# Performance work log

Measured on AMD Instinct MI355X. Metric: run time of the kernel, lower is better.

Reference implementation:

```python
import jax, jax.numpy as jnp
import numpy as np

D = 65
CHUNK = 64
K = 64
SCALE = D ** (-0.5)

def gelu(x):
    return jax.nn.gelu(x, approximate=False)  # torch nn.GELU default is exact erf

def setup_inputs() -> dict:
    key = jax.random.key(0)
    ks = jax.random.split(key, 16)
    B, N = 32, 16384
    s = SCALE
    return {
        "x": jax.random.normal(ks[0], (B, N, D), jnp.float32),
        # query_gen: Linear(D,D) -> GELU -> Linear(D, K*D)
        "Wq1": jax.random.normal(ks[1], (D, D), jnp.float32) * s,
        "bq1": jnp.zeros((D,), jnp.float32),
        "Wq2": jax.random.normal(ks[2], (D, K * D), jnp.float32) * s,
        "bq2": jnp.zeros((K * D,), jnp.float32),
        "Wk": jax.random.normal(ks[3], (D, D), jnp.float32) * s,
        "bk": jnp.zeros((D,), jnp.float32),
        "Wv": jax.random.normal(ks[4], (D, D), jnp.float32) * s,
        "bv": jnp.zeros((D,), jnp.float32),
        "cross_q": jax.random.normal(ks[5], (1, D), jnp.float32) * s,
        "pos_enc": jax.random.normal(ks[6], (1, CHUNK, D), jnp.float32) * s,
        "Wr": jax.random.normal(ks[7], (D, D), jnp.float32) * (1.0 / np.sqrt(D)),
        "br": jnp.zeros((D,), jnp.float32),
        "gamma": jnp.ones((D,), jnp.float32),
        "beta": jnp.zeros((D,), jnp.float32),
    }

def reference(x, Wq1, bq1, Wq2, bq2, Wk, bk, Wv, bv, cross_q, pos_enc, Wr, br, gamma, beta):
    B, N, d = x.shape
    nb = N // CHUNK  # N chosen divisible by CHUNK -> mask is all True, pad branch skipped

    # global average (mask all-ones => plain mean over N)
    gavg = jnp.mean(x, axis=1)  # [B, D]

    # queries: MLP on global average, reshape to [B, K, D], scaled
    q = (gelu(gavg @ Wq1 + bq1) @ Wq2 + bq2).reshape(B, K, d) * SCALE

    # keys / values: Linear + GELU, chunked, + positional encoding per chunk
    keys = gelu(x @ Wk + bk).reshape(B, nb, CHUNK, d) + pos_enc[None]      # [B,nb,C,D]
    values = gelu(x @ Wv + bv).reshape(B, nb, CHUNK, d) + pos_enc[None]    # [B,nb,C,D]

    # block-local attention (mask is all-True, masked_fill is a no-op)
    scores = jnp.einsum('bkd,bncd->bnkc', q, keys) * SCALE                 # [B,nb,K,C]
    w = jax.nn.softmax(scores, axis=-1)                                    # dropout = eval-mode identity
    blk = jnp.einsum('bnkc,bncd->bnkd', w, values)                         # [B,nb,K,D]
    blk = jnp.transpose(blk, (0, 2, 1, 3))                                 # [B,K,nb,D]

    # cross-block attention with a single learned query
    cs = jnp.einsum('d,bknd->bkn', cross_q[0], blk) * SCALE                # [B,K,nb]
    cw = jax.nn.softmax(cs, axis=-1)
    compressed = jnp.einsum('bkn,bknd->bkd', cw, blk)                      # [B,K,D]

    # residual + LayerNorm
    compressed = compressed + (gavg @ Wr + br)[:, None, :]
    mu = jnp.mean(compressed, axis=-1, keepdims=True)
    var = jnp.var(compressed, axis=-1, keepdims=True)
    return (compressed - mu) * jax.lax.rsqrt(var + 1e-5) * gamma + beta
```

## Files before the change

kernel.cpp:

```cpp
#include <hip/hip_runtime.h>
#include <hip/hip_bf16.h>

#define BATCH 32
#define NSEQ  16384
#define DDIM  65
#define CHUNK 64
#define KQ    64
#define NBLK  256
#define SCALE 0.12403473458920847f

typedef __bf16 bf16x8 __attribute__((ext_vector_type(8)));
typedef float  f32x4  __attribute__((ext_vector_type(4)));
#define MFMA16(a, b, c) __builtin_amdgcn_mfma_f32_16x16x32_bf16(a, b, c, 0, 0, 0)

__device__ __forceinline__ float gelu_exact(float v) {
    return 0.5f * v * (1.0f + erff(v * 0.7071067811865476f));
}

__device__ __forceinline__ float gelu_tanh(float x) {
    float x2 = x * x;
    float t  = 0.7978845608028654f * x * fmaf(0.044715f, x2, 1.0f);
    float e  = __expf(2.0f * t);
    float th = 1.0f - 2.0f * __builtin_amdgcn_rcpf(e + 1.0f);
    return 0.5f * x * (1.0f + th);
}

__global__ __launch_bounds__(256) void k_prep(const float* __restrict__ Wk,
                                              const float* __restrict__ Wv,
                                              __bf16* __restrict__ WkT,
                                              __bf16* __restrict__ WvT) {
    int i = blockIdx.x * 256 + threadIdx.x;
    if (i >= 2 * 80 * 64) return;
    int m = i / 5120;
    int j = i - m * 5120;
    int d = j >> 6, e = j & 63;
    const float* W = m ? Wv : Wk;
    __bf16* T = m ? WvT : WkT;
    T[(size_t)d * 64 + e] = (d < DDIM) ? (__bf16)W[e * DDIM + d] : (__bf16)0.0f;
}

__global__ __launch_bounds__(256) void k_gavg(const float* __restrict__ x,
                                              float* __restrict__ partial) {
    const int s = blockIdx.x;
    const int b = blockIdx.y;
    const int tid = threadIdx.x;
    const int w = tid >> 6, lane = tid & 63;
    const float* xb = x + (size_t)b * NSEQ * DDIM;
    const int n0 = s * 256;
    float acc = 0.f, acce = 0.f;
    #pragma unroll 4
    for (int i = 0; i < 64; ++i) {
        const float* row = xb + (size_t)(n0 + w + i * 4) * DDIM;
        acc  += row[lane];
        acce += row[64];
    }
    __shared__ float part[4][DDIM];
    part[w][lane] = acc;
    if (lane == 0) part[w][64] = acce;
    __syncthreads();
    if (tid < DDIM) {
        partial[((size_t)b * 64 + s) * DDIM + tid] =
            part[0][tid] + part[1][tid] + part[2][tid] + part[3][tid];
    }
}

__global__ __launch_bounds__(256) void k_qgen1(const float* __restrict__ partial,
    const float* __restrict__ Wq1, const float* __restrict__ bq1,
    const float* __restrict__ Wr,  const float* __restrict__ br,
    float* __restrict__ h_out, float* __restrict__ r_out) {
    const int b = blockIdx.x, tid = threadIdx.x;
    __shared__ float g[DDIM];
    if (tid < DDIM) {
        float a = 0.f;
        const float* p = partial + (size_t)b * 64 * DDIM + tid;
        #pragma unroll 8
        for (int s = 0; s < 64; ++s) a += p[s * DDIM];
        g[tid] = a * (1.0f / 16384.0f);
    }
    __syncthreads();
    if (tid < DDIM) {
        float a = bq1[tid];
        for (int e = 0; e < DDIM; ++e) a += g[e] * Wq1[e * DDIM + tid];
        h_out[b * DDIM + tid] = gelu_exact(a);
    } else if (tid >= 128 && tid < 128 + DDIM) {
        const int d = tid - 128;
        float a = br[d];
        for (int e = 0; e < DDIM; ++e) a += g[e] * Wr[e * DDIM + d];
        r_out[b * DDIM + d] = a;
    }
}

__global__ __launch_bounds__(256) void k_qgen2(const float* __restrict__ h_in,
    const float* __restrict__ Wq2, const float* __restrict__ bq2,
    __bf16* __restrict__ qbf, float* __restrict__ q64) {
    const int b = blockIdx.y, tid = threadIdx.x;
    const int o = blockIdx.x * 256 + tid;
    __shared__ float h[DDIM];
    if (tid < DDIM) h[tid] = h_in[b * DDIM + tid];
    __syncthreads();
    if (o >= KQ * DDIM) return;
    float a = bq2[o];
    #pragma unroll 13
    for (int e = 0; e < DDIM; ++e) a += h[e] * Wq2[e * (KQ * DDIM) + o];
    a *= SCALE;
    const int k = o / DDIM, d = o - k * DDIM;
    if (d < 64) qbf[(size_t)b * 4096 + k * 64 + d] = (__bf16)a;
    else        q64[b * 64 + k] = a;
}

__global__ __launch_bounds__(256, 5) void k_attn(const float* __restrict__ x,
    const __bf16* __restrict__ qbf, const float* __restrict__ q64,
    const __bf16* __restrict__ WkT, const __bf16* __restrict__ WvT,
    const float* __restrict__ Wk, const float* __restrict__ bkb,
    const float* __restrict__ Wv, const float* __restrict__ bvb,
    const float* __restrict__ pos, const float* __restrict__ cq,
    __bf16* __restrict__ blk_out, float* __restrict__ cs_out) {
    const int nb = blockIdx.x;
    const int b  = blockIdx.y;
    const int tid = threadIdx.x;
    const int lane = tid & 63, w = tid >> 6;
    const int l16 = lane & 15, quad = lane >> 4;

    __shared__ __align__(16) __bf16 xsP[64 * 72];
    __shared__ __align__(16) __bf16 keys[64 * 72];
    __shared__ __align__(16) __bf16 valsT[64 * 72];
    __shared__ float vals64[64];
    __shared__ float xs64[64];

    {
        const int c = tid >> 2, g = tid & 3;
        const float* xrow = x + ((size_t)b * NSEQ + (size_t)nb * CHUNK + c) * DDIM;
        __bf16* dst = xsP + c * 72;
        #pragma unroll
        for (int j = 0; j < 16; ++j)
            dst[g + 4 * j] = (__bf16)xrow[g + 4 * j];
        if (g == 0) xs64[c] = xrow[64];
    }
    __syncthreads();

    {
        const __bf16* arow = xsP + (w * 16 + l16) * 72 + quad * 8;
        bf16x8 a0 = *(const bf16x8*)arow;
        bf16x8 a1 = *(const bf16x8*)(arow + 32);
        f32x4 ak[5], av[5];
        const f32x4 z = {0.f, 0.f, 0.f, 0.f};
        #pragma unroll
        for (int nt = 0; nt < 5; ++nt) {
            const __bf16* bkr = WkT + (nt * 16 + l16) * 64 + quad * 8;
            const __bf16* bvr = WvT + (nt * 16 + l16) * 64 + quad * 8;
            ak[nt] = MFMA16(a0, *(const bf16x8*)bkr, z);
            ak[nt] = MFMA16(a1, *(const bf16x8*)(bkr + 32), ak[nt]);
            av[nt] = MFMA16(a0, *(const bf16x8*)bvr, z);
            av[nt] = MFMA16(a1, *(const bf16x8*)(bvr + 32), av[nt]);
        }
        float xe[4];
        #pragma unroll
        for (int r = 0; r < 4; ++r) xe[r] = xs64[w * 16 + quad * 4 + r];
        #pragma unroll
        for (int nt = 0; nt < 5; ++nt) {
            const int d = nt * 16 + l16;
            if (d <= 64) {
                const float wk64d = Wk[64 * DDIM + d];
                const float wv64d = Wv[64 * DDIM + d];
                const float bkd = bkb[d], bvd = bvb[d];
                #pragma unroll
                for (int r = 0; r < 4; ++r) {
                    const int c = w * 16 + quad * 4 + r;
                    const float pv = pos[c * DDIM + d];
                    const float kvv = gelu_tanh(ak[nt][r] + xe[r] * wk64d + bkd) + pv;
                    const float vvv = gelu_tanh(av[nt][r] + xe[r] * wv64d + bvd) + pv;
                    keys[c * 72 + d] = (__bf16)kvv;
                    if (d < 64) valsT[d * 72 + c] = (__bf16)vvv;
                    else        vals64[c] = vvv;
                }
            }
        }
    }
    __syncthreads();

    float csr[4];
    {
        const __bf16* aq = qbf + (size_t)b * 4096 + (w * 16 + l16) * 64 + quad * 8;
        bf16x8 qa0 = *(const bf16x8*)aq;
        bf16x8 qa1 = *(const bf16x8*)(aq + 32);
        const f32x4 z = {0.f, 0.f, 0.f, 0.f};
        float st[4][4];
        #pragma unroll
        for (int nt = 0; nt < 4; ++nt) {
            const __bf16* kb = keys + (nt * 16 + l16) * 72 + quad * 8;
            f32x4 sacc = MFMA16(qa0, *(const bf16x8*)kb, z);
            sacc = MFMA16(qa1, *(const bf16x8*)(kb + 32), sacc);
            const float k64c = (float)keys[(nt * 16 + l16) * 72 + 64];
            #pragma unroll
            for (int r = 0; r < 4; ++r) st[nt][r] = sacc[r] * SCALE + 0.f * k64c;
            #pragma unroll
            for (int r = 0; r < 4; ++r)
                st[nt][r] = sacc[r];
            #pragma unroll
            for (int r = 0; r < 4; ++r)
                st[nt][r] = fmaf(q64[b * 64 + w * 16 + quad * 4 + r], k64c,
                                 st[nt][r]) * SCALE;
        }
        float mr[4], sum[4], inv[4];
        #pragma unroll
        for (int r = 0; r < 4; ++r) {
            float m = fmaxf(fmaxf(st[0][r], st[1][r]), fmaxf(st[2][r], st[3][r]));
            m = fmaxf(m, __shfl_xor(m, 1));
            m = fmaxf(m, __shfl_xor(m, 2));
            m = fmaxf(m, __shfl_xor(m, 4));
            m = fmaxf(m, __shfl_xor(m, 8));
            mr[r] = m;
            sum[r] = 0.f;
        }
        #pragma unroll
        for (int nt = 0; nt < 4; ++nt)
            #pragma unroll
            for (int r = 0; r < 4; ++r) {
                st[nt][r] = __expf(st[nt][r] - mr[r]);
                sum[r] += st[nt][r];
            }
        #pragma unroll
        for (int r = 0; r < 4; ++r) {
            float s = sum[r];
            s += __shfl_xor(s, 1);
            s += __shfl_xor(s, 2);
            s += __shfl_xor(s, 4);
            s += __shfl_xor(s, 8);
            inv[r] = __builtin_amdgcn_rcpf(s);
        }
        #pragma unroll
        for (int nt = 0; nt < 4; ++nt)
            #pragma unroll
            for (int r = 0; r < 4; ++r)
                xsP[(w * 16 + quad * 4 + r) * 72 + nt * 16 + l16] =
                    (__bf16)(st[nt][r] * inv[r]);
        float v64l[4];
        #pragma unroll
        for (int nt = 0; nt < 4; ++nt) v64l[nt] = vals64[nt * 16 + l16];
        const float cq64 = cq[64];
        #pragma unroll
        for (int r = 0; r < 4; ++r) {
            float o = st[0][r] * v64l[0];
            o = fmaf(st[1][r], v64l[1], o);
            o = fmaf(st[2][r], v64l[2], o);
            o = fmaf(st[3][r], v64l[3], o);
            o += __shfl_xor(o, 1);
            o += __shfl_xor(o, 2);
            o += __shfl_xor(o, 4);
            o += __shfl_xor(o, 8);
            csr[r] = 0.f;
            if (l16 == 0) {
                const float o64 = o * inv[r];
                const int k = w * 16 + quad * 4 + r;
                blk_out[(((size_t)b * KQ + k) * NBLK + nb) * DDIM + 64] =
                    (__bf16)o64;
                csr[r] = o64 * cq64;
            }
        }
    }
    __syncthreads();

    {
        const __bf16* pr = xsP + (w * 16 + l16) * 72 + quad * 8;
        bf16x8 pa0 = *(const bf16x8*)pr;
        bf16x8 pa1 = *(const bf16x8*)(pr + 32);
        const f32x4 z = {0.f, 0.f, 0.f, 0.f};
        #pragma unroll
        for (int nt = 0; nt < 4; ++nt) {
            const __bf16* vb = valsT + (nt * 16 + l16) * 72 + quad * 8;
            f32x4 o = MFMA16(pa0, *(const bf16x8*)vb, z);
            o = MFMA16(pa1, *(const bf16x8*)(vb + 32), o);
            const int d = nt * 16 + l16;
            const float cqd = cq[d];
            #pragma unroll
            for (int r = 0; r < 4; ++r) {
                const int k = w * 16 + quad * 4 + r;
                blk_out[(((size_t)b * KQ + k) * NBLK + nb) * DDIM + d] =
                    (__bf16)o[r];
                csr[r] = fmaf(o[r], cqd, csr[r]);
            }
        }
        #pragma unroll
        for (int r = 0; r < 4; ++r) {
            float v = csr[r];
            v += __shfl_xor(v, 1);
            v += __shfl_xor(v, 2);
            v += __shfl_xor(v, 4);
            v += __shfl_xor(v, 8);
            if (l16 == 0) {
                const int k = w * 16 + quad * 4 + r;
                cs_out[((size_t)b * KQ + k) * NBLK + nb] = v * SCALE;
            }
        }
    }
}

__global__ __launch_bounds__(256) void k_cross(
    const __bf16* __restrict__ blk, const float* __restrict__ cs,
    const float* __restrict__ r, const float* __restrict__ gamma,
    const float* __restrict__ beta, float* __restrict__ out) {
    const int bk_ = blockIdx.x;
    const int b = bk_ >> 6;
    const int tid = threadIdx.x;
    const int w = tid >> 6, lane = tid & 63;

    __shared__ float ew[NBLK];
    __shared__ float red[4][DDIM];
    __shared__ float vv[DDIM];
    __shared__ float wredA[4];
    __shared__ float stats[2];

    const float v = cs[(size_t)bk_ * NBLK + tid];
    float m = v;
    for (int off = 32; off; off >>= 1) m = fmaxf(m, __shfl_down(m, off));
    if (lane == 0) wredA[w] = m;
    __syncthreads();
    m = fmaxf(fmaxf(wredA[0], wredA[1]), fmaxf(wredA[2], wredA[3]));
    const float e = __expf(v - m);
    ew[tid] = e;
    float s = e;
    for (int off = 32; off; off >>= 1) s += __shfl_down(s, off);
    __syncthreads();
    if (lane == 0) wredA[w] = s;
    __syncthreads();
    const float inv = 1.0f / (wredA[0] + wredA[1] + wredA[2] + wredA[3]);

    const __bf16* base = blk + (size_t)bk_ * NBLK * DDIM;
    float acc = 0.f, acce = 0.f;
    #pragma unroll 4
    for (int i = 0; i < 64; ++i) {
        const int n = w + i * 4;
        const __bf16* row = base + n * DDIM;
        const float wgt = ew[n];
        acc  += wgt * (float)row[lane];
        acce += wgt * (float)row[64];
    }
    red[w][lane] = acc;
    if (lane == 0) red[w][64] = acce;
    __syncthreads();
    if (tid < DDIM) {
        vv[tid] = (red[0][tid] + red[1][tid] + red[2][tid] + red[3][tid]) * inv
                  + r[b * DDIM + tid];
    }
    __syncthreads();
    if (tid < 64) {
        float a  = vv[tid] + (tid == 0 ? vv[64] : 0.f);
        float sq = vv[tid] * vv[tid] + (tid == 0 ? vv[64] * vv[64] : 0.f);
        for (int off = 32; off; off >>= 1) {
            a  += __shfl_down(a, off);
            sq += __shfl_down(sq, off);
        }
        if (tid == 0) {
            const float mu  = a * (1.0f / DDIM);
            const float var = sq * (1.0f / DDIM) - mu * mu;
            stats[0] = mu;
            stats[1] = rsqrtf(var + 1e-5f);
        }
    }
    __syncthreads();
    if (tid < DDIM) {
        out[(size_t)bk_ * DDIM + tid] =
            (vv[tid] - stats[0]) * stats[1] * gamma[tid] + beta[tid];
    }
}

extern "C" void kernel_launch(void* const* d_in, const int* in_sizes, int n_in,
                              void* d_out, int out_size, void* d_ws, size_t ws_size,
                              hipStream_t stream) {
    const float* x    = (const float*)d_in[0];
    const float* Wq1  = (const float*)d_in[1];
    const float* bq1  = (const float*)d_in[2];
    const float* Wq2  = (const float*)d_in[3];
    const float* bq2  = (const float*)d_in[4];
    const float* Wk   = (const float*)d_in[5];
    const float* bk   = (const float*)d_in[6];
    const float* Wv   = (const float*)d_in[7];
    const float* bv   = (const float*)d_in[8];
    const float* cq   = (const float*)d_in[9];
    const float* pos  = (const float*)d_in[10];
    const float* Wr   = (const float*)d_in[11];
    const float* br   = (const float*)d_in[12];
    const float* gamma= (const float*)d_in[13];
    const float* beta = (const float*)d_in[14];
    float* out = (float*)d_out;

    char* w8 = (char*)d_ws;
    float*  partial = (float*)w8;
    float*  rres    = (float*)(w8 + 532480);
    float*  q64     = (float*)(w8 + 540800);
    float*  hbuf    = (float*)(w8 + 548992);
    float*  cs      = (float*)(w8 + 557312);
    __bf16* qbf     = (__bf16*)(w8 + 2654464);
    __bf16* WkT     = (__bf16*)(w8 + 2916608);
    __bf16* WvT     = (__bf16*)(w8 + 2926848);
    __bf16* blk     = (__bf16*)(w8 + 2937088);

    k_prep<<<40, 256, 0, stream>>>(Wk, Wv, WkT, WvT);
    k_gavg<<<dim3(64, BATCH), 256, 0, stream>>>(x, partial);
    k_qgen1<<<BATCH, 256, 0, stream>>>(partial, Wq1, bq1, Wr, br, hbuf, rres);
    k_qgen2<<<dim3(17, BATCH), 256, 0, stream>>>(hbuf, Wq2, bq2, qbf, q64);
    k_attn<<<dim3(NBLK, BATCH), 256, 0, stream>>>(x, qbf, q64, WkT, WvT,
                                                  Wk, bk, Wv, bv, pos, cq,
                                                  blk, cs);
    k_cross<<<BATCH * KQ, 256, 0, stream>>>(blk, cs, rres, gamma, beta, out);
}
```

Measured before the change: 378.3 us.

## Pre-convert x to swizzled bf16 and restructure attention kernel with async LDS loads

The global-average kernel now also writes x as a bf16, XOR-swizzled 64-column copy plus a separate fp32 column 64. The attention kernel pulls this with global_load_lds straight into LDS and uses swizzled unpadded LDS tiles with transposed MFMA operand order so each lane owns one query row, which removes cross-lane softmax reductions and one barrier. The block output layout becomes [b][nb][k] with stride 68 so stores are vectorized, and occupancy is raised to 6. In exchange there is an extra bf16 write and read of x through global memory, and k_cross now reads strided rows.

```diff
diff --git a/kernel.cpp b/kernel.cpp
--- a/kernel.cpp
+++ b/kernel.cpp
@@ -8,8 +8,10 @@
 #define KQ    64
 #define NBLK  256
 #define SCALE 0.12403473458920847f
+#define BSTRIDE 68
 
 typedef __bf16 bf16x8 __attribute__((ext_vector_type(8)));
+typedef __bf16 bf16x4 __attribute__((ext_vector_type(4)));
 typedef float  f32x4  __attribute__((ext_vector_type(4)));
 #define MFMA16(a, b, c) __builtin_amdgcn_mfma_f32_16x16x32_bf16(a, b, c, 0, 0, 0)
 
@@ -23,6 +25,12 @@
     float e  = __expf(2.0f * t);
     float th = 1.0f - 2.0f * __builtin_amdgcn_rcpf(e + 1.0f);
     return 0.5f * x * (1.0f + th);
+}
+
+__device__ __forceinline__ void load_lds16(const void* g, void* l) {
+    __builtin_amdgcn_global_load_lds(
+        (const __attribute__((address_space(1))) unsigned int*)g,
+        (__attribute__((address_space(3))) unsigned int*)l, 16, 0, 0);
 }
 
 __global__ __launch_bounds__(256) void k_prep(const float* __restrict__ Wk,
@@ -40,7 +48,9 @@
 }
 
 __global__ __launch_bounds__(256) void k_gavg(const float* __restrict__ x,
-                                              float* __restrict__ partial) {
+                                              float* __restrict__ partial,
+                                              __bf16* __restrict__ xbf,
+                                              float* __restrict__ x64g) {
     const int s = blockIdx.x;
     const int b = blockIdx.y;
     const int tid = threadIdx.x;
@@ -50,9 +60,16 @@
     float acc = 0.f, acce = 0.f;
     #pragma unroll 4
     for (int i = 0; i < 64; ++i) {
-        const float* row = xb + (size_t)(n0 + w + i * 4) * DDIM;
-        acc  += row[lane];
-        acce += row[64];
+        const int n = n0 + w + i * 4;
+        const float* row = xb + (size_t)n * DDIM;
+        const float v = row[lane];
+        acc += v;
+        xbf[((size_t)b * NSEQ + n) * 64 + (lane ^ ((n & 7) << 3))] = (__bf16)v;
+        if (lane == 0) {
+            const float ve = row[64];
+            acce += ve;
+            x64g[(size_t)b * NSEQ + n] = ve;
+        }
     }
     __shared__ float part[4][DDIM];
     part[w][lane] = acc;
@@ -108,8 +125,9 @@
     else        q64[b * 64 + k] = a;
 }
 
-__global__ __launch_bounds__(256, 5) void k_attn(const float* __restrict__ x,
-    const __bf16* __restrict__ qbf, const float* __restrict__ q64,
+__global__ __launch_bounds__(256, 6) void k_attn(
+    const __bf16* __restrict__ xbf, const float* __restrict__ x64g,
+    const __bf16* __restrict__ qbf, const float* __restrict__ q64g,
     const __bf16* __restrict__ WkT, const __bf16* __restrict__ WvT,
     const float* __restrict__ Wk, const float* __restrict__ bkb,
     const float* __restrict__ Wv, const float* __restrict__ bvb,
@@ -121,176 +139,188 @@
     const int lane = tid & 63, w = tid >> 6;
     const int l16 = lane & 15, quad = lane >> 4;
 
-    __shared__ __align__(16) __bf16 xsP[64 * 72];
-    __shared__ __align__(16) __bf16 keys[64 * 72];
-    __shared__ __align__(16) __bf16 valsT[64 * 72];
-    __shared__ float vals64[64];
+    __shared__ __align__(16) __bf16 xP[64 * 64];
+    __shared__ __align__(16) __bf16 keysL[64 * 64];
+    __shared__ __align__(16) __bf16 valsT[64 * 64];
+    __shared__ __align__(16) __bf16 kcol64[64];
+    __shared__ __align__(16) __bf16 vcol64[64];
     __shared__ float xs64[64];
 
+    const int krow = w * 16 + l16;
+    const __bf16* qr = qbf + (size_t)b * 4096 + krow * 64 + quad * 8;
+    bf16x8 q0 = *(const bf16x8*)qr;
+    bf16x8 q1 = *(const bf16x8*)(qr + 32);
+    const float q64k = q64g[b * 64 + krow];
+
     {
-        const int c = tid >> 2, g = tid & 3;
-        const float* xrow = x + ((size_t)b * NSEQ + (size_t)nb * CHUNK + c) * DDIM;
-        __bf16* dst = xsP + c * 72;
-        #pragma unroll
-        for (int j = 0; j < 16; ++j)
-            dst[g + 4 * j] = (__bf16)xrow[g + 4 * j];
-        if (g == 0) xs64[c] = xrow[64];
+        const char* xg = (const char*)(xbf + ((size_t)b * NSEQ + (size_t)nb * CHUNK) * 64);
+        char* lp = (char*)xP;
+        #pragma unroll
+        for (int j = 0; j < 2; ++j) {
+            const int o = j * 4096 + w * 1024;
+            load_lds16(xg + o + lane * 16, lp + o);
+        }
+        if (tid < 64) xs64[tid] = x64g[(size_t)b * NSEQ + (size_t)nb * CHUNK + tid];
     }
     __syncthreads();
 
     {
-        const __bf16* arow = xsP + (w * 16 + l16) * 72 + quad * 8;
-        bf16x8 a0 = *(const bf16x8*)arow;
-        bf16x8 a1 = *(const bf16x8*)(arow + 32);
-        f32x4 ak[5], av[5];
+        const int crow = w * 16 + l16;
+        const int sw_c = (crow & 7) << 4;
+        const char* xrow = (const char*)xP + crow * 128;
+        bf16x8 x0 = *(const bf16x8*)(xrow + ((quad * 16) ^ sw_c));
+        bf16x8 x1 = *(const bf16x8*)(xrow + ((quad * 16 + 64) ^ sw_c));
+        const float xe_c = xs64[crow];
         const f32x4 z = {0.f, 0.f, 0.f, 0.f};
+
+        f32x4 kacc[5];
+        #pragma unroll
+        for (int mt = 0; mt < 5; ++mt) {
+            const __bf16* wr = WkT + (mt * 16 + l16) * 64 + quad * 8;
+            kacc[mt] = MFMA16(*(const bf16x8*)wr, x0, z);
+            kacc[mt] = MFMA16(*(const bf16x8*)(wr + 32), x1, kacc[mt]);
+        }
+        #pragma unroll
+        for (int mt = 0; mt < 4; ++mt) {
+            const int d0 = mt * 16 + quad * 4;
+            bf16x4 kv;
+            #pragma unroll
+            for (int r = 0; r < 4; ++r) {
+                const int d = d0 + r;
+                const float pre = kacc[mt][r] + xe_c * Wk[64 * DDIM + d] + bkb[d];
+                kv[r] = (__bf16)(gelu_tanh(pre) + pos[crow * DDIM + d]);
+            }
+            *(bf16x4*)((char*)keysL + crow * 128 + ((d0 * 2) ^ sw_c)) = kv;
+        }
+        if (quad == 0) {
+            const float pre = kacc[4][0] + xe_c * Wk[64 * DDIM + 64] + bkb[64];
+            kcol64[crow] = (__bf16)(gelu_tanh(pre) + pos[crow * DDIM + 64]);
+        }
+
+        f32x4 vacc[5];
         #pragma unroll
         for (int nt = 0; nt < 5; ++nt) {
-            const __bf16* bkr = WkT + (nt * 16 + l16) * 64 + quad * 8;
-            const __bf16* bvr = WvT + (nt * 16 + l16) * 64 + quad * 8;
-            ak[nt] = MFMA16(a0, *(const bf16x8*)bkr, z);
-            ak[nt] = MFMA16(a1, *(const bf16x8*)(bkr + 32), ak[nt]);
-            av[nt] = MFMA16(a0, *(const bf16x8*)bvr, z);
-            av[nt] = MFMA16(a1, *(const bf16x8*)(bvr + 32), av[nt]);
-        }
-        float xe[4];
-        #pragma unroll
-        for (int r = 0; r < 4; ++r) xe[r] = xs64[w * 16 + quad * 4 + r];
-        #pragma unroll
-        for (int nt = 0; nt < 5; ++nt) {
+            const __bf16* wr = WvT + (nt * 16 + l16) * 64 + quad * 8;
+            vacc[nt] = MFMA16(x0, *(const bf16x8*)wr, z);
+            vacc[nt] = MFMA16(x1, *(const bf16x8*)(wr + 32), vacc[nt]);
+        }
+        const int cv0 = w * 16 + quad * 4;
+        float xe4[4];
+        #pragma unroll
+        for (int r = 0; r < 4; ++r) xe4[r] = xs64[cv0 + r];
+        #pragma unroll
+        for (int nt = 0; nt < 4; ++nt) {
             const int d = nt * 16 + l16;
-            if (d <= 64) {
-                const float wk64d = Wk[64 * DDIM + d];
-                const float wv64d = Wv[64 * DDIM + d];
-                const float bkd = bkb[d], bvd = bvb[d];
-                #pragma unroll
-                for (int r = 0; r < 4; ++r) {
-                    const int c = w * 16 + quad * 4 + r;
-                    const float pv = pos[c * DDIM + d];
-                    const float kvv = gelu_tanh(ak[nt][r] + xe[r] * wk64d + bkd) + pv;
-                    const float vvv = gelu_tanh(av[nt][r] + xe[r] * wv64d + bvd) + pv;
-                    keys[c * 72 + d] = (__bf16)kvv;
-                    if (d < 64) valsT[d * 72 + c] = (__bf16)vvv;
-                    else        vals64[c] = vvv;
-                }
+            const float wv64d = Wv[64 * DDIM + d], bvd = bvb[d];
+            bf16x4 vv;
+            #pragma unroll
+            for (int r = 0; r < 4; ++r) {
+                const float pre = vacc[nt][r] + xe4[r] * wv64d + bvd;
+                vv[r] = (__bf16)(gelu_tanh(pre) + pos[(cv0 + r) * DDIM + d]);
             }
-        }
-    }
-    __syncthreads();
-
-    float csr[4];
+            *(bf16x4*)((char*)valsT + d * 128 + ((cv0 * 2) ^ ((d & 7) << 4))) = vv;
+        }
+        if (l16 == 0) {
+            const float wv64d = Wv[64 * DDIM + 64], bvd = bvb[64];
+            bf16x4 vv;
+            #pragma unroll
+            for (int r = 0; r < 4; ++r) {
+                const float pre = vacc[4][r] + xe4[r] * wv64d + bvd;
+                vv[r] = (__bf16)(gelu_tanh(pre) + pos[(cv0 + r) * DDIM + 64]);
+            }
+            *(bf16x4*)((char*)vcol64 + cv0 * 2) = vv;
+        }
+    }
+    __syncthreads();
+
+    float inv_k, o64n;
     {
-        const __bf16* aq = qbf + (size_t)b * 4096 + (w * 16 + l16) * 64 + quad * 8;
-        bf16x8 qa0 = *(const bf16x8*)aq;
-        bf16x8 qa1 = *(const bf16x8*)(aq + 32);
         const f32x4 z = {0.f, 0.f, 0.f, 0.f};
         float st[4][4];
         #pragma unroll
-        for (int nt = 0; nt < 4; ++nt) {
-            const __bf16* kb = keys + (nt * 16 + l16) * 72 + quad * 8;
-            f32x4 sacc = MFMA16(qa0, *(const bf16x8*)kb, z);
-            sacc = MFMA16(qa1, *(const bf16x8*)(kb + 32), sacc);
-            const float k64c = (float)keys[(nt * 16 + l16) * 72 + 64];
-            #pragma unroll
-            for (int r = 0; r < 4; ++r) st[nt][r] = sacc[r] * SCALE + 0.f * k64c;
+        for (int mt = 0; mt < 4; ++mt) {
+            const int cA = mt * 16 + l16;
+            const char* kr = (const char*)keysL + cA * 128;
+            const int swc = (cA & 7) << 4;
+            f32x4 s = MFMA16(*(const bf16x8*)(kr + ((quad * 16) ^ swc)), q0, z);
+            s = MFMA16(*(const bf16x8*)(kr + ((quad * 16 + 64) ^ swc)), q1, s);
+            bf16x4 k4 = *(const bf16x4*)((const char*)kcol64 + (mt * 16 + quad * 4) * 2);
             #pragma unroll
             for (int r = 0; r < 4; ++r)
-                st[nt][r] = sacc[r];
-            #pragma unroll
-            for (int r = 0; r < 4; ++r)
-                st[nt][r] = fmaf(q64[b * 64 + w * 16 + quad * 4 + r], k64c,
-                                 st[nt][r]) * SCALE;
-        }
-        float mr[4], sum[4], inv[4];
-        #pragma unroll
-        for (int r = 0; r < 4; ++r) {
-            float m = fmaxf(fmaxf(st[0][r], st[1][r]), fmaxf(st[2][r], st[3][r]));
-            m = fmaxf(m, __shfl_xor(m, 1));
-            m = fmaxf(m, __shfl_xor(m, 2));
-            m = fmaxf(m, __shfl_xor(m, 4));
-            m = fmaxf(m, __shfl_xor(m, 8));
-            mr[r] = m;
-            sum[r] = 0.f;
-        }
-        #pragma unroll
-        for (int nt = 0; nt < 4; ++nt)
+                st[mt][r] = fmaf(q64k, (float)k4[r], s[r]) * SCALE;
+        }
+        float m = st[0][0];
+        #pragma unroll
+        for (int mt = 0; mt < 4; ++mt)
+            #pragma unroll
+            for (int r = 0; r < 4; ++r) m = fmaxf(m, st[mt][r]);
+        m = fmaxf(m, __shfl_xor(m, 16));
+        m = fmaxf(m, __shfl_xor(m, 32));
+        float sum = 0.f;
+        #pragma unroll
+        for (int mt = 0; mt < 4; ++mt)
             #pragma unroll
             for (int r = 0; r < 4; ++r) {
-                st[nt][r] = __expf(st[nt][r] - mr[r]);
-                sum[r] += st[nt][r];
+                st[mt][r] = __expf(st[mt][r] - m);
+                sum += st[mt][r];
             }
-        #pragma unroll
-        for (int r = 0; r < 4; ++r) {
-            float s = sum[r];
-            s += __shfl_xor(s, 1);
-            s += __shfl_xor(s, 2);
-            s += __shfl_xor(s, 4);
-            s += __shfl_xor(s, 8);
-            inv[r] = __builtin_amdgcn_rcpf(s);
-        }
-        #pragma unroll
-        for (int nt = 0; nt < 4; ++nt)
-            #pragma unroll
-            for (int r = 0; r < 4; ++r)
-                xsP[(w * 16 + quad * 4 + r) * 72 + nt * 16 + l16] =
-                    (__bf16)(st[nt][r] * inv[r]);
-        float v64l[4];
-        #pragma unroll
-        for (int nt = 0; nt < 4; ++nt) v64l[nt] = vals64[nt * 16 + l16];
-        const float cq64 = cq[64];
-        #pragma unroll
-        for (int r = 0; r < 4; ++r) {
-            float o = st[0][r] * v64l[0];
-            o = fmaf(st[1][r], v64l[1], o);
-            o = fmaf(st[2][r], v64l[2], o);
-            o = fmaf(st[3][r], v64l[3], o);
-            o += __shfl_xor(o, 1);
-            o += __shfl_xor(o, 2);
-            o += __shfl_xor(o, 4);
-            o += __shfl_xor(o, 8);
-            csr[r] = 0.f;
-            if (l16 == 0) {
-                const float o64 = o * inv[r];
-                const int k = w * 16 + quad * 4 + r;
-                blk_out[(((size_t)b * KQ + k) * NBLK + nb) * DDIM + 64] =
-                    (__bf16)o64;
-                csr[r] = o64 * cq64;
+        sum += __shfl_xor(sum, 16);
+        sum += __shfl_xor(sum, 32);
+        inv_k = __builtin_amdgcn_rcpf(sum);
+
+        const int swk = (krow & 7) << 4;
+        char* prow = (char*)xP + krow * 128;
+        #pragma unroll
+        for (int mt = 0; mt < 4; ++mt) {
+            bf16x4 p4;
+            #pragma unroll
+            for (int r = 0; r < 4; ++r) p4[r] = (__bf16)st[mt][r];
+            *(bf16x4*)(prow + (((mt * 16 + quad * 4) * 2) ^ swk)) = p4;
+        }
+
+        float o = 0.f;
+        #pragma unroll
+        for (int mt = 0; mt < 4; ++mt) {
+            bf16x4 v4 = *(const bf16x4*)((const char*)vcol64 + (mt * 16 + quad * 4) * 2);
+            #pragma unroll
+            for (int r = 0; r < 4; ++r) o = fmaf(st[mt][r], (float)v4[r], o);
+        }
+        o += __shfl_xor(o, 16);
+        o += __shfl_xor(o, 32);
+        o64n = o * inv_k;
+        if (quad == 0)
+            blk_out[(((size_t)b * NBLK + nb) * KQ + krow) * BSTRIDE + 64] = (__bf16)o64n;
+    }
+
+    {
+        const f32x4 z = {0.f, 0.f, 0.f, 0.f};
+        const int swk = (krow & 7) << 4;
+        const char* prow = (const char*)xP + krow * 128;
+        bf16x8 p0 = *(const bf16x8*)(prow + ((quad * 16) ^ swk));
+        bf16x8 p1 = *(const bf16x8*)(prow + ((quad * 16 + 64) ^ swk));
+        const size_t obase = (((size_t)b * NBLK + nb) * KQ + krow) * BSTRIDE;
+        float csp = 0.f;
+        #pragma unroll
+        for (int mt = 0; mt < 4; ++mt) {
+            const int dA = mt * 16 + l16;
+            const char* vr = (const char*)valsT + dA * 128;
+            const int swd = (dA & 7) << 4;
+            f32x4 o = MFMA16(*(const bf16x8*)(vr + ((quad * 16) ^ swd)), p0, z);
+            o = MFMA16(*(const bf16x8*)(vr + ((quad * 16 + 64) ^ swd)), p1, o);
+            const int d0 = mt * 16 + quad * 4;
+            bf16x4 o4;
+            #pragma unroll
+            for (int r = 0; r < 4; ++r) {
+                o4[r] = (__bf16)(o[r] * inv_k);
+                csp = fmaf(o[r], cq[d0 + r], csp);
             }
-        }
-    }
-    __syncthreads();
-
-    {
-        const __bf16* pr = xsP + (w * 16 + l16) * 72 + quad * 8;
-        bf16x8 pa0 = *(const bf16x8*)pr;
-        bf16x8 pa1 = *(const bf16x8*)(pr + 32);
-        const f32x4 z = {0.f, 0.f, 0.f, 0.f};
-        #pragma unroll
-        for (int nt = 0; nt < 4; ++nt) {
-            const __bf16* vb = valsT + (nt * 16 + l16) * 72 + quad * 8;
-            f32x4 o = MFMA16(pa0, *(const bf16x8*)vb, z);
-            o = MFMA16(pa1, *(const bf16x8*)(vb + 32), o);
-            const int d = nt * 16 + l16;
-            const float cqd = cq[d];
-            #pragma unroll
-            for (int r = 0; r < 4; ++r) {
-                const int k = w * 16 + quad * 4 + r;
-                blk_out[(((size_t)b * KQ + k) * NBLK + nb) * DDIM + d] =
-                    (__bf16)o[r];
-                csr[r] = fmaf(o[r], cqd, csr[r]);
-            }
-        }
-        #pragma unroll
-        for (int r = 0; r < 4; ++r) {
-            float v = csr[r];
-            v += __shfl_xor(v, 1);
-            v += __shfl_xor(v, 2);
-            v += __shfl_xor(v, 4);
-            v += __shfl_xor(v, 8);
-            if (l16 == 0) {
-                const int k = w * 16 + quad * 4 + r;
-                cs_out[((size_t)b * KQ + k) * NBLK + nb] = v * SCALE;
-            }
+            *(bf16x4*)((char*)blk_out + (obase + d0) * 2) = o4;
+        }
+        csp += __shfl_xor(csp, 16);
+        csp += __shfl_xor(csp, 32);
+        if (quad == 0) {
+            const float cs = (csp * inv_k + cq[64] * o64n) * SCALE;
+            cs_out[((size_t)b * KQ + krow) * NBLK + nb] = cs;
         }
     }
 }
@@ -301,6 +331,7 @@
     const float* __restrict__ beta, float* __restrict__ out) {
     const int bk_ = blockIdx.x;
     const int b = bk_ >> 6;
+    const int k = bk_ & 63;
     const int tid = threadIdx.x;
     const int w = tid >> 6, lane = tid & 63;
 
@@ -325,12 +356,12 @@
     __syncthreads();
     const float inv = 1.0f / (wredA[0] + wredA[1] + wredA[2] + wredA[3]);
 
-    const __bf16* base = blk + (size_t)bk_ * NBLK * DDIM;
+    const __bf16* base = blk + ((size_t)b * NBLK * KQ + k) * BSTRIDE;
     float acc = 0.f, acce = 0.f;
     #pragma unroll 4
     for (int i = 0; i < 64; ++i) {
         const int n = w + i * 4;
-        const __bf16* row = base + n * DDIM;
+        const __bf16* row = base + (size_t)n * (KQ * BSTRIDE);
         const float wgt = ew[n];
         acc  += wgt * (float)row[lane];
         acce += wgt * (float)row[64];
@@ -393,13 +424,15 @@
     __bf16* qbf     = (__bf16*)(w8 + 2654464);
     __bf16* WkT     = (__bf16*)(w8 + 2916608);
     __bf16* WvT     = (__bf16*)(w8 + 2926848);
-    __bf16* blk     = (__bf16*)(w8 + 2937088);
+    float*  x64     = (float*)(w8 + 2937088);
+    __bf16* xbf     = (__bf16*)(w8 + 5034240);
+    __bf16* blk     = (__bf16*)(w8 + 72143104);
 
     k_prep<<<40, 256, 0, stream>>>(Wk, Wv, WkT, WvT);
-    k_gavg<<<dim3(64, BATCH), 256, 0, stream>>>(x, partial);
+    k_gavg<<<dim3(64, BATCH), 256, 0, stream>>>(x, partial, xbf, x64);
     k_qgen1<<<BATCH, 256, 0, stream>>>(partial, Wq1, bq1, Wr, br, hbuf, rres);
     k_qgen2<<<dim3(17, BATCH), 256, 0, stream>>>(hbuf, Wq2, bq2, qbf, q64);
-    k_attn<<<dim3(NBLK, BATCH), 256, 0, stream>>>(x, qbf, q64, WkT, WvT,
+    k_attn<<<dim3(NBLK, BATCH), 256, 0, stream>>>(xbf, x64, qbf, q64, WkT, WvT,
                                                   Wk, bk, Wv, bv, pos, cq,
                                                   blk, cs);
     k_cross<<<BATCH * KQ, 256, 0, stream>>>(blk, cs, rres, gamma, beta, out);
```

After: 432.3 us. 1.14x slower.
